# Kernel tuning notes

Measured on AMD Instinct MI355X. Metric: run time of the kernel, lower is better.

## Reference

```python
import jax, jax.numpy as jnp
import numpy as np

FP8_MAX = 448.0  # e4m3 max (use_e4m3=True)
FP8_DTYPE = jnp.float8_e4m3fn


def _quant_dequant(t):
    # scale = fp8_max / clamp(amax, 1e-12); quantize with clamp + fp8 cast; dequantize with 1/scale
    amax = jnp.maximum(jnp.abs(t).max(), 1e-12)
    scale = FP8_MAX / amax
    q = jnp.clip(t * scale, -FP8_MAX, FP8_MAX).astype(FP8_DTYPE)
    return q.astype(jnp.float32) * (1.0 / scale)


def setup_inputs() -> dict:
    key = jax.random.key(0)
    k1, k2 = jax.random.split(key)
    x = jax.random.normal(k1, (8, 2048, 4096), dtype=jnp.float32)
    weight = jax.random.normal(k2, (4096, 4096), dtype=jnp.float32) * 0.02  # (K, N)
    return {"x": x, "weight": weight}


def reference(x, weight):
    bsz, seqlen, K = x.shape
    x2d = x.reshape(-1, K)                    # (M, K)
    a32 = _quant_dequant(x2d)                 # fp8 round-trip of activations
    w32_t = _quant_dequant(weight.T)          # fp8 round-trip of transposed weight (N, K)
    out = a32 @ w32_t.T                       # (M, N) fp32 GEMM
    return out.astype(x.dtype).reshape(bsz, seqlen, -1)
```

## Files before the change

### kernel.cpp

```cpp
#include <hip/hip_runtime.h>
#include <hip/hip_bf16.h>

#define M_DIM 16384
#define N_DIM 4096
#define K_DIM 4096
#define FP8_MAX 448.0f

#define BM 256
#define BN 256
#define NK64 (K_DIM / 64)
#define NKT NK64

typedef float f32x16 __attribute__((ext_vector_type(16)));
typedef int i32x4 __attribute__((ext_vector_type(4)));
typedef int i32x8 __attribute__((ext_vector_type(8)));


__global__ void init_amax_kernel(unsigned* amax) {
    if (threadIdx.x < 2) amax[threadIdx.x] = 0u;
}

__global__ void amax_kernel(const float* __restrict__ p, long n4,
                            unsigned* __restrict__ out) {
    float m = 0.f;
    const float4* p4 = (const float4*)p;
    for (long i = (long)blockIdx.x * blockDim.x + threadIdx.x; i < n4;
         i += (long)gridDim.x * blockDim.x) {
        float4 v = p4[i];
        m = fmaxf(m, fmaxf(fmaxf(fabsf(v.x), fabsf(v.y)),
                           fmaxf(fabsf(v.z), fabsf(v.w))));
    }
#pragma unroll
    for (int off = 32; off > 0; off >>= 1)
        m = fmaxf(m, __shfl_down(m, off));
    __shared__ float smax[4];
    int lane = threadIdx.x & 63, wid = threadIdx.x >> 6;
    if (lane == 0) smax[wid] = m;
    __syncthreads();
    if (threadIdx.x == 0) {
        float bm = fmaxf(fmaxf(smax[0], smax[1]), fmaxf(smax[2], smax[3]));
        atomicMax(out, __float_as_uint(bm));
    }
}

__device__ __forceinline__ unsigned pack4(float4 v, float s) {
    float a = fminf(fmaxf(v.x * s, -FP8_MAX), FP8_MAX);
    float b = fminf(fmaxf(v.y * s, -FP8_MAX), FP8_MAX);
    float c = fminf(fmaxf(v.z * s, -FP8_MAX), FP8_MAX);
    float d = fminf(fmaxf(v.w * s, -FP8_MAX), FP8_MAX);
    int p = 0;
    p = __builtin_amdgcn_cvt_pk_fp8_f32(a, b, p, false);
    p = __builtin_amdgcn_cvt_pk_fp8_f32(c, d, p, true);
    return (unsigned)p;
}

__global__ void quant_x_kernel(const float* __restrict__ x,
                               unsigned char* __restrict__ q,
                               const unsigned* __restrict__ amax) {
    float scale = FP8_MAX / fmaxf(__uint_as_float(amax[0]), 1e-12f);
    int m32 = blockIdx.x;
    int t = threadIdx.x;
    int lane = t & 63;
    int g = t >> 6;
    int m = m32 * 32 + (lane & 31);
    int kh = lane >> 5;
    const float* rp = x + (long)m * K_DIM;
    unsigned char* ob = q + (long)m32 * NK64 * 2048;
#pragma unroll
    for (int it = 0; it < 16; ++it) {
        int k64 = it * 4 + g;
        int kb = k64 * 64 + kh * 32;
        float4 v0 = *(const float4*)&rp[kb];
        float4 v1 = *(const float4*)&rp[kb + 4];
        float4 v2 = *(const float4*)&rp[kb + 8];
        float4 v3 = *(const float4*)&rp[kb + 12];
        float4 v4 = *(const float4*)&rp[kb + 16];
        float4 v5 = *(const float4*)&rp[kb + 20];
        float4 v6 = *(const float4*)&rp[kb + 24];
        float4 v7 = *(const float4*)&rp[kb + 28];
        uint4 o0, o1;
        o0.x = pack4(v0, scale); o0.y = pack4(v1, scale);
        o0.z = pack4(v2, scale); o0.w = pack4(v3, scale);
        o1.x = pack4(v4, scale); o1.y = pack4(v5, scale);
        o1.z = pack4(v6, scale); o1.w = pack4(v7, scale);
        *(uint4*)&ob[(long)k64 * 2048 + lane * 16] = o0;
        *(uint4*)&ob[(long)k64 * 2048 + 1024 + lane * 16] = o1;
    }
}

__global__ void quant_wt_kernel(const float* __restrict__ w,
                                unsigned char* __restrict__ qw,
                                const unsigned* __restrict__ amax) {
    __shared__ unsigned tile[64][17];
    float scale = FP8_MAX / fmaxf(__uint_as_float(amax[1]), 1e-12f);
    int b = blockIdx.x;
    int bk = b & 63, bn = b >> 6;
    int k0 = bk * 64, n0 = bn * 64;
    int t = threadIdx.x;
#pragma unroll
    for (int pass = 0; pass < 4; ++pass) {
        int idx = pass * 256 + t;
        int k = idx >> 4, nw = idx & 15;
        float4 v = *(const float4*)&w[(long)(k0 + k) * N_DIM + n0 + nw * 4];
        tile[k][nw] = pack4(v, scale);
    }
    __syncthreads();
    int lane = t & 63, g = t >> 6;
    int n32 = g >> 1, h = g & 1;
    int nl = n32 * 32 + (lane & 31);
    int word = nl >> 2, sh = (nl & 3) * 8;
    int kb = (lane >> 5) * 32 + h * 16;
    uint4 o;
    unsigned* ow = (unsigned*)&o;
#pragma unroll
    for (int wd = 0; wd < 4; ++wd) {
        unsigned acc = 0;
#pragma unroll
        for (int j = 0; j < 4; ++j)
            acc |= ((tile[kb + wd * 4 + j][word] >> sh) & 0xffu) << (8 * j);
        ow[wd] = acc;
    }
    long gn32 = (long)(n0 >> 5) + n32;
    *(uint4*)&qw[(gn32 * NK64 + bk) * 2048 + h * 1024 + lane * 16] = o;
}

__device__ __forceinline__ void stage_q(const unsigned char* __restrict__ Aseg,
                                        const unsigned char* __restrict__ Bseg,
                                        unsigned char* stbuf, int tid, int kt, int r) {
    int c = r * 512 + tid;
    int f = (c >> 7) & 7;
    int q = c & 127;
    const unsigned char* src =
        ((c < 1024) ? Aseg : Bseg) + ((long)f * NK64 + kt) * 2048 + q * 16;
    __builtin_amdgcn_global_load_lds(
        (const __attribute__((address_space(1))) void*)src,
        (__attribute__((address_space(3))) void*)(stbuf + c * 16), 16, 0, 0);
}

__device__ __forceinline__ i32x8 comb(i32x4 lo, i32x4 hi) {
    return __builtin_shufflevector(lo, hi, 0, 1, 2, 3, 4, 5, 6, 7);
}

template <int VW, bool STG, bool NEXT>
__device__ __forceinline__ void tile_step(
    unsigned char* sbase, const unsigned char* __restrict__ Aseg,
    const unsigned char* __restrict__ Bseg, int kt, int tid, int lane,
    int wm, int wn, i32x4 (&ca)[4][2], i32x4 (&cb)[2][2],
    i32x4 (&na)[4][2], i32x4 (&nb)[2][2], f32x16 (&acc)[4][2]) {
    if constexpr (VW == 4)
        asm volatile("s_waitcnt vmcnt(4) lgkmcnt(0)" ::: "memory");
    else if constexpr (VW == 0)
        asm volatile("s_waitcnt vmcnt(0) lgkmcnt(0)" ::: "memory");
    if constexpr (VW >= 0) {
        __builtin_amdgcn_sched_barrier(0);
        __builtin_amdgcn_s_barrier();
        __builtin_amdgcn_sched_barrier(0);
    }

    if constexpr (NEXT) {
        const unsigned char* nbuf = sbase + (size_t)((kt + 1) & 3) * 32768;
        const unsigned char* nAl = nbuf + wm * 4 * 2048;
        const unsigned char* nBl = nbuf + 16384 + wn * 2 * 2048;
#pragma unroll
        for (int i = 0; i < 4; ++i) {
            na[i][0] = *(const i32x4*)(nAl + i * 2048 + lane * 16);
            na[i][1] = *(const i32x4*)(nAl + i * 2048 + 1024 + lane * 16);
        }
#pragma unroll
        for (int j = 0; j < 2; ++j) {
            nb[j][0] = *(const i32x4*)(nBl + j * 2048 + lane * 16);
            nb[j][1] = *(const i32x4*)(nBl + j * 2048 + 1024 + lane * 16);
        }
    }
    if constexpr (STG) {
        unsigned char* stbuf = sbase + (size_t)((kt + 3) & 3) * 32768;
        stage_q(Aseg, Bseg, stbuf, tid, kt + 3, 0);
        stage_q(Aseg, Bseg, stbuf, tid, kt + 3, 1);
        stage_q(Aseg, Bseg, stbuf, tid, kt + 3, 2);
        stage_q(Aseg, Bseg, stbuf, tid, kt + 3, 3);
    }
    __builtin_amdgcn_sched_barrier(0);
    __builtin_amdgcn_s_setprio(1);
#pragma unroll
    for (int i = 0; i < 4; ++i)
        acc[i][0] = __builtin_amdgcn_mfma_scale_f32_32x32x64_f8f6f4(
            comb(ca[i][0], ca[i][1]), comb(cb[0][0], cb[0][1]), acc[i][0],
            0, 0, 0, 0x7f7f7f7f, 0, 0x7f7f7f7f);
#pragma unroll
    for (int i = 0; i < 4; ++i)
        acc[i][1] = __builtin_amdgcn_mfma_scale_f32_32x32x64_f8f6f4(
            comb(ca[i][0], ca[i][1]), comb(cb[1][0], cb[1][1]), acc[i][1],
            0, 0, 0, 0x7f7f7f7f, 0, 0x7f7f7f7f);
    __builtin_amdgcn_s_setprio(0);
}

__global__ __launch_bounds__(512, 2) void gemm_fp8_kernel(
    const unsigned char* __restrict__ qa, const unsigned char* __restrict__ qw,
    float* __restrict__ out, const unsigned* __restrict__ amax) {
    __shared__ unsigned char lds[4][32768];

    int b = blockIdx.x;
    int swz = (b & 7) * 128 + (b >> 3);
    int bm = swz >> 4;
    int bn = swz & 15;

    int tid = threadIdx.x;
    int lane = tid & 63;
    int w = tid >> 6;
    int wm = w >> 2, wn = w & 3;

    f32x16 acc[4][2];
#pragma unroll
    for (int i = 0; i < 4; ++i)
#pragma unroll
        for (int j = 0; j < 2; ++j) acc[i][j] = (f32x16)0.f;

    const unsigned char* Aseg = qa + (long)(bm * 8) * NK64 * 2048;
    const unsigned char* Bseg = qw + (long)(bn * 8) * NK64 * 2048;
    unsigned char* sbase = &lds[0][0];

#pragma unroll
    for (int pt = 0; pt < 3; ++pt)
#pragma unroll
        for (int r = 0; r < 4; ++r)
            stage_q(Aseg, Bseg, sbase + (size_t)pt * 32768, tid, pt, r);
    asm volatile("s_waitcnt vmcnt(8)" ::: "memory");
    __builtin_amdgcn_s_barrier();

    i32x4 A0[4][2], B0[2][2], A1[4][2], B1[2][2];
    {
        const unsigned char* Al = sbase + wm * 4 * 2048;
        const unsigned char* Bl = sbase + 16384 + wn * 2 * 2048;
#pragma unroll
        for (int i = 0; i < 4; ++i) {
            A0[i][0] = *(const i32x4*)(Al + i * 2048 + lane * 16);
            A0[i][1] = *(const i32x4*)(Al + i * 2048 + 1024 + lane * 16);
        }
#pragma unroll
        for (int j = 0; j < 2; ++j) {
            B0[j][0] = *(const i32x4*)(Bl + j * 2048 + lane * 16);
            B0[j][1] = *(const i32x4*)(Bl + j * 2048 + 1024 + lane * 16);
        }
    }

#pragma unroll 1
    for (int kt = 0; kt < 60; kt += 2) {
        tile_step<4, true, true>(sbase, Aseg, Bseg, kt, tid, lane, wm, wn,
                                 A0, B0, A1, B1, acc);
        tile_step<4, true, true>(sbase, Aseg, Bseg, kt + 1, tid, lane, wm, wn,
                                 A1, B1, A0, B0, acc);
    }
    tile_step<4, true, true>(sbase, Aseg, Bseg, 60, tid, lane, wm, wn,
                             A0, B0, A1, B1, acc);
    tile_step<4, false, true>(sbase, Aseg, Bseg, 61, tid, lane, wm, wn,
                              A1, B1, A0, B0, acc);
    tile_step<0, false, true>(sbase, Aseg, Bseg, 62, tid, lane, wm, wn,
                              A0, B0, A1, B1, acc);
    tile_step<-1, false, false>(sbase, Aseg, Bseg, 63, tid, lane, wm, wn,
                                A1, B1, A0, B0, acc);

    float ax = fmaxf(__uint_as_float(amax[0]), 1e-12f);
    float aw = fmaxf(__uint_as_float(amax[1]), 1e-12f);
    float s = ax * aw * (1.0f / (FP8_MAX * FP8_MAX));

    long m0 = (long)bm * BM + wm * 128;
    long n0 = (long)bn * BN + wn * 64;
    int col = lane & 31;
    int rbase = 4 * (lane >> 5);
#pragma unroll
    for (int i = 0; i < 4; ++i)
#pragma unroll
        for (int j = 0; j < 2; ++j)
#pragma unroll
            for (int reg = 0; reg < 16; ++reg) {
                int row = (reg & 3) + 8 * (reg >> 2) + rbase;
                out[(m0 + i * 32 + row) * N_DIM + n0 + j * 32 + col] =
                    acc[i][j][reg] * s;
            }
}

extern "C" void kernel_launch(void* const* d_in, const int* in_sizes, int n_in,
                              void* d_out, int out_size, void* d_ws, size_t ws_size,
                              hipStream_t stream) {
    const float* x = (const float*)d_in[0];
    const float* wgt = (const float*)d_in[1];
    float* out = (float*)d_out;

    unsigned* amax = (unsigned*)d_ws;
    unsigned char* qa = (unsigned char*)d_ws + 256;
    unsigned char* qw = qa + (long)M_DIM * K_DIM;

    init_amax_kernel<<<1, 64, 0, stream>>>(amax);
    amax_kernel<<<2048, 256, 0, stream>>>(x, (long)M_DIM * K_DIM / 4, amax + 0);
    amax_kernel<<<1024, 256, 0, stream>>>(wgt, (long)K_DIM * N_DIM / 4, amax + 1);
    quant_x_kernel<<<M_DIM / 32, 256, 0, stream>>>(x, qa, amax);
    quant_wt_kernel<<<(K_DIM / 64) * (N_DIM / 64), 256, 0, stream>>>(wgt, qw, amax);

    dim3 grid((M_DIM / BM) * (N_DIM / BN));
    gemm_fp8_kernel<<<grid, 512, 0, stream>>>(qa, qw, out, amax);
}
```

Measured before the change: 460.5 us.

## Load B fragments directly from global into registers, stage only A in LDS

```diff
diff --git a/kernel.cpp b/kernel.cpp
--- a/kernel.cpp
+++ b/kernel.cpp
@@ -124,14 +124,13 @@
     *(uint4*)&qw[(gn32 * NK64 + bk) * 2048 + h * 1024 + lane * 16] = o;
 }
 
-__device__ __forceinline__ void stage_q(const unsigned char* __restrict__ Aseg,
-                                        const unsigned char* __restrict__ Bseg,
-                                        unsigned char* stbuf, int tid, int kt, int r) {
+__device__ __forceinline__ void stage_qA(const unsigned char* __restrict__ Aseg,
+                                         unsigned char* stbuf, int tid, int kt,
+                                         int r) {
     int c = r * 512 + tid;
-    int f = (c >> 7) & 7;
+    int f = c >> 7;
     int q = c & 127;
-    const unsigned char* src =
-        ((c < 1024) ? Aseg : Bseg) + ((long)f * NK64 + kt) * 2048 + q * 16;
+    const unsigned char* src = Aseg + ((long)f * NK64 + kt) * 2048 + q * 16;
     __builtin_amdgcn_global_load_lds(
         (const __attribute__((address_space(1))) void*)src,
         (__attribute__((address_space(3))) void*)(stbuf + c * 16), 16, 0, 0);
@@ -141,51 +140,75 @@
     return __builtin_shufflevector(lo, hi, 0, 1, 2, 3, 4, 5, 6, 7);
 }
 
-template <int VW, bool STG, bool NEXT>
+#define SB() __builtin_amdgcn_sched_barrier(0)
+
+template <int VW, bool STG, bool GB, bool NEXT>
 __device__ __forceinline__ void tile_step(
     unsigned char* sbase, const unsigned char* __restrict__ Aseg,
-    const unsigned char* __restrict__ Bseg, int kt, int tid, int lane,
-    int wm, int wn, i32x4 (&ca)[4][2], i32x4 (&cb)[2][2],
+    const unsigned char* __restrict__ Bw, int kt, int tid, int lane,
+    int wm, i32x4 (&ca)[4][2], i32x4 (&cb)[2][2],
     i32x4 (&na)[4][2], i32x4 (&nb)[2][2], f32x16 (&acc)[4][2]) {
-    if constexpr (VW == 4)
-        asm volatile("s_waitcnt vmcnt(4) lgkmcnt(0)" ::: "memory");
-    else if constexpr (VW == 0)
-        asm volatile("s_waitcnt vmcnt(0) lgkmcnt(0)" ::: "memory");
     if constexpr (VW >= 0) {
+        if constexpr (VW == 2)
+            asm volatile("s_waitcnt vmcnt(2) lgkmcnt(0)" ::: "memory");
+        else
+            asm volatile("s_waitcnt vmcnt(0) lgkmcnt(0)" ::: "memory");
         __builtin_amdgcn_sched_barrier(0);
         __builtin_amdgcn_s_barrier();
         __builtin_amdgcn_sched_barrier(0);
     }
-
+    const unsigned char* nAl =
+        sbase + (size_t)((kt + 1) & 3) * 16384 + wm * 4 * 2048 + lane * 16;
+    unsigned char* stbuf = sbase + (size_t)((kt + 3) & 3) * 16384;
+    const unsigned char* Bn = Bw + (long)(kt + 1) * 2048 + lane * 16;
+
+    __builtin_amdgcn_s_setprio(1);
     if constexpr (NEXT) {
-        const unsigned char* nbuf = sbase + (size_t)((kt + 1) & 3) * 32768;
-        const unsigned char* nAl = nbuf + wm * 4 * 2048;
-        const unsigned char* nBl = nbuf + 16384 + wn * 2 * 2048;
-#pragma unroll
-        for (int i = 0; i < 4; ++i) {
-            na[i][0] = *(const i32x4*)(nAl + i * 2048 + lane * 16);
-            na[i][1] = *(const i32x4*)(nAl + i * 2048 + 1024 + lane * 16);
-        }
-#pragma unroll
-        for (int j = 0; j < 2; ++j) {
-            nb[j][0] = *(const i32x4*)(nBl + j * 2048 + lane * 16);
-            nb[j][1] = *(const i32x4*)(nBl + j * 2048 + 1024 + lane * 16);
-        }
-    }
-    if constexpr (STG) {
-        unsigned char* stbuf = sbase + (size_t)((kt + 3) & 3) * 32768;
-        stage_q(Aseg, Bseg, stbuf, tid, kt + 3, 0);
-        stage_q(Aseg, Bseg, stbuf, tid, kt + 3, 1);
-        stage_q(Aseg, Bseg, stbuf, tid, kt + 3, 2);
-        stage_q(Aseg, Bseg, stbuf, tid, kt + 3, 3);
-    }
-    __builtin_amdgcn_sched_barrier(0);
-    __builtin_amdgcn_s_setprio(1);
-#pragma unroll
-    for (int i = 0; i < 4; ++i)
-        acc[i][0] = __builtin_amdgcn_mfma_scale_f32_32x32x64_f8f6f4(
-            comb(ca[i][0], ca[i][1]), comb(cb[0][0], cb[0][1]), acc[i][0],
-            0, 0, 0, 0x7f7f7f7f, 0, 0x7f7f7f7f);
+        na[0][0] = *(const i32x4*)(nAl + 0 * 2048);
+        na[0][1] = *(const i32x4*)(nAl + 0 * 2048 + 1024);
+    }
+    if constexpr (GB) {
+        nb[0][0] = *(const i32x4*)(Bn);
+        nb[0][1] = *(const i32x4*)(Bn + 1024);
+    }
+    SB();
+    acc[0][0] = __builtin_amdgcn_mfma_scale_f32_32x32x64_f8f6f4(
+        comb(ca[0][0], ca[0][1]), comb(cb[0][0], cb[0][1]), acc[0][0],
+        0, 0, 0, 0x7f7f7f7f, 0, 0x7f7f7f7f);
+    SB();
+    if constexpr (NEXT) {
+        na[1][0] = *(const i32x4*)(nAl + 1 * 2048);
+        na[1][1] = *(const i32x4*)(nAl + 1 * 2048 + 1024);
+    }
+    if constexpr (GB) {
+        nb[1][0] = *(const i32x4*)(Bn + (long)NK64 * 2048);
+        nb[1][1] = *(const i32x4*)(Bn + (long)NK64 * 2048 + 1024);
+    }
+    SB();
+    acc[1][0] = __builtin_amdgcn_mfma_scale_f32_32x32x64_f8f6f4(
+        comb(ca[1][0], ca[1][1]), comb(cb[0][0], cb[0][1]), acc[1][0],
+        0, 0, 0, 0x7f7f7f7f, 0, 0x7f7f7f7f);
+    SB();
+    if constexpr (NEXT) {
+        na[2][0] = *(const i32x4*)(nAl + 2 * 2048);
+        na[2][1] = *(const i32x4*)(nAl + 2 * 2048 + 1024);
+    }
+    if constexpr (STG) stage_qA(Aseg, stbuf, tid, kt + 3, 0);
+    SB();
+    acc[2][0] = __builtin_amdgcn_mfma_scale_f32_32x32x64_f8f6f4(
+        comb(ca[2][0], ca[2][1]), comb(cb[0][0], cb[0][1]), acc[2][0],
+        0, 0, 0, 0x7f7f7f7f, 0, 0x7f7f7f7f);
+    SB();
+    if constexpr (NEXT) {
+        na[3][0] = *(const i32x4*)(nAl + 3 * 2048);
+        na[3][1] = *(const i32x4*)(nAl + 3 * 2048 + 1024);
+    }
+    if constexpr (STG) stage_qA(Aseg, stbuf, tid, kt + 3, 1);
+    SB();
+    acc[3][0] = __builtin_amdgcn_mfma_scale_f32_32x32x64_f8f6f4(
+        comb(ca[3][0], ca[3][1]), comb(cb[0][0], cb[0][1]), acc[3][0],
+        0, 0, 0, 0x7f7f7f7f, 0, 0x7f7f7f7f);
+    SB();
 #pragma unroll
     for (int i = 0; i < 4; ++i)
         acc[i][1] = __builtin_amdgcn_mfma_scale_f32_32x32x64_f8f6f4(
@@ -197,12 +220,11 @@
 __global__ __launch_bounds__(512, 2) void gemm_fp8_kernel(
     const unsigned char* __restrict__ qa, const unsigned char* __restrict__ qw,
     float* __restrict__ out, const unsigned* __restrict__ amax) {
-    __shared__ unsigned char lds[4][32768];
+    __shared__ unsigned char lds[4][16384];
 
     int b = blockIdx.x;
-    int swz = (b & 7) * 128 + (b >> 3);
-    int bm = swz >> 4;
-    int bn = swz & 15;
+    int bn = (b & 7) * 2 + ((b >> 3) & 1);
+    int bm = b >> 4;
 
     int tid = threadIdx.x;
     int lane = tid & 63;
@@ -216,48 +238,53 @@
         for (int j = 0; j < 2; ++j) acc[i][j] = (f32x16)0.f;
 
     const unsigned char* Aseg = qa + (long)(bm * 8) * NK64 * 2048;
-    const unsigned char* Bseg = qw + (long)(bn * 8) * NK64 * 2048;
+    const unsigned char* Bw =
+        qw + (long)(bn * 8 + wn * 2) * NK64 * 2048;
+
     unsigned char* sbase = &lds[0][0];
 
-#pragma unroll
-    for (int pt = 0; pt < 3; ++pt)
-#pragma unroll
-        for (int r = 0; r < 4; ++r)
-            stage_q(Aseg, Bseg, sbase + (size_t)pt * 32768, tid, pt, r);
-    asm volatile("s_waitcnt vmcnt(8)" ::: "memory");
+    i32x4 A0[4][2], B0[2][2], A1[4][2], B1[2][2];
+
+#pragma unroll
+    for (int pt = 0; pt < 3; ++pt) {
+        stage_qA(Aseg, sbase + (size_t)pt * 16384, tid, pt, 0);
+        stage_qA(Aseg, sbase + (size_t)pt * 16384, tid, pt, 1);
+    }
+#pragma unroll
+    for (int j = 0; j < 2; ++j) {
+        B0[j][0] = *(const i32x4*)(Bw + (long)j * NK64 * 2048 + lane * 16);
+        B0[j][1] = *(const i32x4*)(Bw + (long)j * NK64 * 2048 + 1024 + lane * 16);
+    }
+    asm volatile("s_waitcnt vmcnt(4)" ::: "memory");
+    __builtin_amdgcn_sched_barrier(0);
     __builtin_amdgcn_s_barrier();
-
-    i32x4 A0[4][2], B0[2][2], A1[4][2], B1[2][2];
+    __builtin_amdgcn_sched_barrier(0);
     {
-        const unsigned char* Al = sbase + wm * 4 * 2048;
-        const unsigned char* Bl = sbase + 16384 + wn * 2 * 2048;
+        const unsigned char* Al = sbase + wm * 4 * 2048 + lane * 16;
 #pragma unroll
         for (int i = 0; i < 4; ++i) {
-            A0[i][0] = *(const i32x4*)(Al + i * 2048 + lane * 16);
-            A0[i][1] = *(const i32x4*)(Al + i * 2048 + 1024 + lane * 16);
+            A0[i][0] = *(const i32x4*)(Al + i * 2048);
+            A0[i][1] = *(const i32x4*)(Al + i * 2048 + 1024);
         }
-#pragma unroll
-        for (int j = 0; j < 2; ++j) {
-            B0[j][0] = *(const i32x4*)(Bl + j * 2048 + lane * 16);
-            B0[j][1] = *(const i32x4*)(Bl + j * 2048 + 1024 + lane * 16);
-        }
-    }
-
+    }
+    asm volatile("s_waitcnt vmcnt(0) lgkmcnt(0)" ::: "memory");
+    __builtin_amdgcn_sched_barrier(0);
+
+    tile_step<-1, true, true, true>(sbase, Aseg, Bw, 0, tid, lane, wm,
+                                    A0, B0, A1, B1, acc);
 #pragma unroll 1
-    for (int kt = 0; kt < 60; kt += 2) {
-        tile_step<4, true, true>(sbase, Aseg, Bseg, kt, tid, lane, wm, wn,
-                                 A0, B0, A1, B1, acc);
-        tile_step<4, true, true>(sbase, Aseg, Bseg, kt + 1, tid, lane, wm, wn,
-                                 A1, B1, A0, B0, acc);
-    }
-    tile_step<4, true, true>(sbase, Aseg, Bseg, 60, tid, lane, wm, wn,
-                             A0, B0, A1, B1, acc);
-    tile_step<4, false, true>(sbase, Aseg, Bseg, 61, tid, lane, wm, wn,
-                              A1, B1, A0, B0, acc);
-    tile_step<0, false, true>(sbase, Aseg, Bseg, 62, tid, lane, wm, wn,
-                              A0, B0, A1, B1, acc);
-    tile_step<-1, false, false>(sbase, Aseg, Bseg, 63, tid, lane, wm, wn,
-                                A1, B1, A0, B0, acc);
+    for (int kt = 1; kt < 61; kt += 2) {
+        tile_step<2, true, true, true>(sbase, Aseg, Bw, kt, tid, lane, wm,
+                                       A1, B1, A0, B0, acc);
+        tile_step<2, (true), true, true>(sbase, Aseg, Bw, kt + 1, tid, lane, wm,
+                                         A0, B0, A1, B1, acc);
+    }
+    tile_step<2, false, true, true>(sbase, Aseg, Bw, 61, tid, lane, wm,
+                                    A1, B1, A0, B0, acc);
+    tile_step<0, false, true, true>(sbase, Aseg, Bw, 62, tid, lane, wm,
+                                    A0, B0, A1, B1, acc);
+    tile_step<0, false, false, false>(sbase, Aseg, Bw, 63, tid, lane, wm,
+                                      A1, B1, A0, B0, acc);
 
     float ax = fmaxf(__uint_as_float(amax[0]), 1e-12f);
     float aw = fmaxf(__uint_as_float(amax[1]), 1e-12f);
```

After: 489.5 us. 1.06x slower.
